# Performance work log

Hardware: AMD Instinct MI355X
Metric: run time of the kernel (lower is better)

The kernel has to match this reference:

```python
import jax, jax.numpy as jnp
import numpy as np

EPS = 1e-6
N_HEADS = 128
QK_NOPE = 128
QK_ROPE = 64
KV_RANK = 512

def rmsnorm(x, gamma):
    var = jnp.mean(jnp.square(x), axis=-1, keepdims=True)
    return x * jax.lax.rsqrt(var + EPS) * gamma

def apply_rope(x, cos, sin):
    # x: [..., D], cos/sin broadcastable to x; rotate-half convention
    x1, x2 = jnp.split(x, 2, axis=-1)
    rot = jnp.concatenate([-x2, x1], axis=-1)
    return x * cos + rot * sin

def setup_inputs() -> dict:
    key = jax.random.key(0)
    ks = jax.random.split(key, 6)
    T, H = 4096, 7168
    inp = {
        "token_x": jax.random.normal(ks[0], (T, H), jnp.float32),
        "wq_a": jax.random.normal(ks[1], (H, 1536), jnp.float32) * 0.02,
        "wq_b": jax.random.normal(ks[2], (1536, N_HEADS * (QK_NOPE + QK_ROPE)), jnp.float32) * 0.02,
        "wkv": jax.random.normal(ks[3], (H, KV_RANK + QK_ROPE), jnp.float32) * 0.02,
        "rope_cos": jax.random.uniform(ks[4], (T, QK_ROPE), jnp.float32, -1.0, 1.0),
        "rope_sin": jax.random.uniform(ks[5], (T, QK_ROPE), jnp.float32, -1.0, 1.0),
        "gamma_cq": jnp.ones((1536,), jnp.float32),
        "gamma_ckv": jnp.ones((KV_RANK,), jnp.float32),
    }
    return inp

def reference(token_x, wq_a, wq_b, wkv, rope_cos, rope_sin, gamma_cq, gamma_ckv):
    T = token_x.shape[0]
    # Query path: down-proj -> RMSNorm -> up-proj -> split -> RoPE on rope part
    cq = rmsnorm(token_x @ wq_a, gamma_cq)                    # [T, 1536]
    q = (cq @ wq_b).reshape(T, N_HEADS, QK_NOPE + QK_ROPE)    # [T, H, 192]
    q_nope, q_rope = q[..., :QK_NOPE], q[..., QK_NOPE:]
    q_rope = apply_rope(q_rope, rope_cos[:, None, :], rope_sin[:, None, :])
    query = jnp.concatenate([q_nope, q_rope], axis=-1)        # [T, H, 192]
    # KV path: joint down-proj -> split latent / rope-key -> RMSNorm + RoPE
    kv = token_x @ wkv                                        # [T, 576]
    ckv = rmsnorm(kv[:, :KV_RANK], gamma_ckv)                 # [T, 512]
    k_rope = apply_rope(kv[:, KV_RANK:], rope_cos, rope_sin)  # [T, 64]
    # Pack outputs into a single array: [T, H*192 + 512 + 64]
    return jnp.concatenate([query.reshape(T, -1), ckv, k_rope], axis=-1)
```

## Files before the change

kernel.cpp:

```cpp
#include <hip/hip_runtime.h>


typedef __attribute__((ext_vector_type(8))) __bf16 bf16x8;
typedef __attribute__((ext_vector_type(4))) float f32x4;

#define OUT_LD 25152

__device__ __forceinline__ unsigned short f2bf(float f) {
  union { float f; unsigned u; } v; v.f = f;
  unsigned r = v.u + 0x7FFFu + ((v.u >> 16) & 1u);
  return (unsigned short)(r >> 16);
}

__device__ __forceinline__ void gload16(const void* g, void* l) {
  __builtin_amdgcn_global_load_lds(
      (__attribute__((address_space(1))) void*)(void*)g,
      (__attribute__((address_space(3))) void*)l, 16, 0, 0);
}

__global__ void cvt_bf16(const float* __restrict__ in, unsigned short* __restrict__ out) {
  size_t i = (size_t)blockIdx.x * 256 + threadIdx.x;
  float4 f = ((const float4*)in)[i];
  ushort4 o;
  o.x = f2bf(f.x); o.y = f2bf(f.y); o.z = f2bf(f.z); o.w = f2bf(f.w);
  ((ushort4*)out)[i] = o;
}

__global__ void transpose_cvt(const float* __restrict__ in, unsigned short* __restrict__ out,
                              int K, int N, int Npad) {
  __shared__ float tile[32][33];
  int k0 = blockIdx.x * 32, n0 = blockIdx.y * 32;
  int tx = threadIdx.x, ty = threadIdx.y;
#pragma unroll
  for (int i = 0; i < 4; ++i) {
    int k = k0 + ty + i * 8;
    int n = n0 + tx;
    tile[ty + i * 8][tx] = (n < N) ? in[(size_t)k * N + n] : 0.f;
  }
  __syncthreads();
#pragma unroll
  for (int i = 0; i < 4; ++i) {
    int n = n0 + ty + i * 8;
    int k = k0 + tx;
    if (n < Npad) out[(size_t)n * K + k] = f2bf(tile[tx][ty + i * 8]);
  }
}

__global__ __launch_bounds__(512, 2) void gemm256(
    const unsigned short* __restrict__ A, const unsigned short* __restrict__ B,
    float* __restrict__ C, int K, int ldc, int Mtiles,
    const float* __restrict__ cs, const float* __restrict__ sn, int rope) {
  __shared__ __attribute__((aligned(128))) char lds[131072];
  const int tid = threadIdx.x;
  const int lane = tid & 63;
  const int wr = (tid >> 6) >> 2;
  const int wc = (tid >> 6) & 3;
  const int NT = K >> 6;

  const int nwg = gridDim.x;
  const int per = nwg >> 3;
  const int bid = blockIdx.x;
  const int swz = (bid & 7) * per + (bid >> 3);
  const int bm = swz % Mtiles, bn = swz / Mtiles;

  const int strow = tid >> 3;
  const int stcolb = (((tid & 7) ^ ((tid >> 3) & 7)) << 4);
  const size_t abase = (size_t)(bm * 256) * K;
  const size_t bbase = (size_t)(bn * 256) * K;

  f32x4 acc[2][2][4][2];
  const f32x4 z4 = {0.f, 0.f, 0.f, 0.f};
#pragma unroll
  for (int a = 0; a < 2; ++a)
#pragma unroll
    for (int b = 0; b < 2; ++b)
#pragma unroll
      for (int c = 0; c < 4; ++c)
#pragma unroll
        for (int d = 0; d < 2; ++d) acc[a][b][c][d] = z4;

#define STAGE_A(kt, bsel, u)                                                          \
  do {                                                                                \
    int row_ = (u) * 64 + strow;                                                      \
    gload16((const char*)(A + abase + (size_t)row_ * K + (size_t)(kt) * 64) + stcolb, \
            lds + (bsel) * 65536 + (u) * 8192 + tid * 16);                            \
  } while (0)
#define STAGE_B(kt, bsel, u)                                                          \
  do {                                                                                \
    int lrow_ = (u) * 64 + strow;                                                     \
    int n_ = ((lrow_ >> 5) & 3) * 64 + ((lrow_ >> 7) & 1) * 32 + (lrow_ & 31);        \
    gload16((const char*)(B + bbase + (size_t)n_ * K + (size_t)(kt) * 64) + stcolb,   \
            lds + (bsel) * 65536 + 32768 + (u) * 8192 + tid * 16);                    \
  } while (0)

#define READ_A(dst, QM, LBASE)                                              \
  do {                                                                      \
    _Pragma("unroll") for (int mf = 0; mf < 4; ++mf)                        \
        _Pragma("unroll") for (int ks = 0; ks < 2; ++ks) {                  \
      int row_ = (QM) * 128 + wr * 64 + mf * 16 + (lane & 15);              \
      int in_ = (ks * 64 + ((lane >> 4) << 4)) ^ ((row_ & 7) << 4);         \
      dst[mf][ks] = *(const bf16x8*)((LBASE) + row_ * 128 + in_);           \
    }                                                                       \
  } while (0)
#define READ_B(dst, QN, LBASE)                                              \
  do {                                                                      \
    _Pragma("unroll") for (int nf = 0; nf < 2; ++nf)                        \
        _Pragma("unroll") for (int ks = 0; ks < 2; ++ks) {                  \
      int c_ = wc * 64 + (QN) * 32 + nf * 16 + (lane & 15);                 \
      int rr_ = ((c_ >> 5) & 1) * 128 + ((c_ >> 6) & 3) * 32 + (c_ & 31);   \
      int in_ = (ks * 64 + ((lane >> 4) << 4)) ^ ((rr_ & 7) << 4);          \
      dst[nf][ks] = *(const bf16x8*)((LBASE) + 32768 + rr_ * 128 + in_);    \
    }                                                                       \
  } while (0)
#define MFMA_Q(QM, QN, AF, BB)                                              \
  do {                                                                      \
    __builtin_amdgcn_s_setprio(1);                                          \
    _Pragma("unroll") for (int mf = 0; mf < 4; ++mf)                        \
        _Pragma("unroll") for (int nf = 0; nf < 2; ++nf)                    \
            _Pragma("unroll") for (int ks = 0; ks < 2; ++ks)                \
                acc[QM][QN][mf][nf] = __builtin_amdgcn_mfma_f32_16x16x32_bf16( \
                    AF[mf][ks], BB[nf][ks], acc[QM][QN][mf][nf], 0, 0, 0);  \
    __builtin_amdgcn_s_setprio(0);                                          \
  } while (0)

  STAGE_A(0, 0, 0); STAGE_A(0, 0, 1); STAGE_A(0, 0, 2); STAGE_A(0, 0, 3);
  STAGE_B(0, 0, 0); STAGE_B(0, 0, 1); STAGE_B(0, 0, 2); STAGE_B(0, 0, 3);
  asm volatile("s_waitcnt vmcnt(0)" ::: "memory");
  __builtin_amdgcn_s_barrier();
  __builtin_amdgcn_sched_barrier(0);

  bf16x8 af0[4][2], af1[4][2], bb0[2][2], bb1[2][2];

  for (int t = 0; t < NT; ++t) {
    const int buf = t & 1;
    const int pb = buf ^ 1;
    const char* Lb = lds + buf * 65536;

    if (t + 1 < NT) {
      STAGE_A(t + 1, pb, 0); STAGE_A(t + 1, pb, 1);
      STAGE_A(t + 1, pb, 2); STAGE_A(t + 1, pb, 3);
      STAGE_B(t + 1, pb, 0); STAGE_B(t + 1, pb, 1);
      STAGE_B(t + 1, pb, 2); STAGE_B(t + 1, pb, 3);
    }
    __builtin_amdgcn_sched_barrier(0);

    READ_A(af0, 0, Lb);
    READ_B(bb0, 0, Lb);
    __builtin_amdgcn_sched_barrier(0);
    READ_B(bb1, 1, Lb);
    __builtin_amdgcn_sched_barrier(0);
    READ_A(af1, 1, Lb);
    __builtin_amdgcn_sched_barrier(0);

    asm volatile("s_waitcnt lgkmcnt(12)" ::: "memory");
    __builtin_amdgcn_sched_barrier(0);
    MFMA_Q(0, 0, af0, bb0);

    asm volatile("s_waitcnt lgkmcnt(8)" ::: "memory");
    __builtin_amdgcn_sched_barrier(0);
    MFMA_Q(0, 1, af0, bb1);

    asm volatile("s_waitcnt lgkmcnt(0)" ::: "memory");
    __builtin_amdgcn_sched_barrier(0);
    MFMA_Q(1, 1, af1, bb1);
    MFMA_Q(1, 0, af1, bb0);

    asm volatile("s_waitcnt vmcnt(0)" ::: "memory");
    __builtin_amdgcn_s_barrier();
    __builtin_amdgcn_sched_barrier(0);
  }

  const int colbase = bn * 256 + wc * 64;
  const int rbase = bm * 256 + wr * 64 + ((lane >> 4) << 2);
  const bool isrope = rope && ((colbase % 192) == 128);
  if (isrope) {
#pragma unroll
    for (int qm = 0; qm < 2; ++qm)
#pragma unroll
      for (int mf = 0; mf < 4; ++mf)
#pragma unroll
        for (int nf = 0; nf < 2; ++nf) {
          int i_ = nf * 16 + (lane & 15);
#pragma unroll
          for (int r = 0; r < 4; ++r) {
            int trow = rbase + qm * 128 + mf * 16 + r;
            float c1 = cs[trow * 64 + i_], s1 = sn[trow * 64 + i_];
            float c2 = cs[trow * 64 + 32 + i_], s2 = sn[trow * 64 + 32 + i_];
            float a = acc[qm][0][mf][nf][r], b = acc[qm][1][mf][nf][r];
            C[(size_t)trow * ldc + colbase + i_] = a * c1 - b * s1;
            C[(size_t)trow * ldc + colbase + 32 + i_] = b * c2 + a * s2;
          }
        }
  } else {
#pragma unroll
    for (int qm = 0; qm < 2; ++qm)
#pragma unroll
      for (int qn = 0; qn < 2; ++qn)
#pragma unroll
        for (int mf = 0; mf < 4; ++mf)
#pragma unroll
          for (int nf = 0; nf < 2; ++nf)
#pragma unroll
            for (int r = 0; r < 4; ++r) {
              int trow = rbase + qm * 128 + mf * 16 + r;
              C[(size_t)trow * ldc + colbase + qn * 32 + nf * 16 + (lane & 15)] =
                  acc[qm][qn][mf][nf][r];
            }
  }
#undef MFMA_Q
#undef READ_B
#undef READ_A
#undef STAGE_B
#undef STAGE_A
}

__global__ __launch_bounds__(256, 2) void gemm128(
    const unsigned short* __restrict__ A, const unsigned short* __restrict__ B,
    float* __restrict__ C, int K, int ldc, int Nvalid) {
  __shared__ __attribute__((aligned(128))) unsigned short As[128 * 32];
  __shared__ __attribute__((aligned(128))) unsigned short Bs[128 * 32];
  const int tid = threadIdx.x;
  const int lane = tid & 63;
  const int wid = tid >> 6;
  const int wr = wid >> 1, wc = wid & 1;
  const int bm = blockIdx.y, bn = blockIdx.x;
  const size_t abase = (size_t)bm * 128 * K;
  const size_t bbase = (size_t)bn * 128 * K;

  f32x4 acc[4][4];
  const f32x4 zero4 = {0.f, 0.f, 0.f, 0.f};
#pragma unroll
  for (int m = 0; m < 4; ++m)
#pragma unroll
    for (int n = 0; n < 4; ++n) acc[m][n] = zero4;

  const int r0 = tid >> 2;
  const int c0 = (tid & 3) * 8;

  for (int k0 = 0; k0 < K; k0 += 32) {
    gload16(A + abase + (size_t)r0 * K + k0 + c0, As + tid * 8);
    gload16(A + abase + (size_t)(r0 + 64) * K + k0 + c0, As + (256 + tid) * 8);
    gload16(B + bbase + (size_t)r0 * K + k0 + c0, Bs + tid * 8);
    gload16(B + bbase + (size_t)(r0 + 64) * K + k0 + c0, Bs + (256 + tid) * 8);
    __syncthreads();
    bf16x8 af[4], bfr[4];
#pragma unroll
    for (int m = 0; m < 4; ++m)
      af[m] = *(const bf16x8*)(As + (wr * 64 + m * 16 + (lane & 15)) * 32 + (lane >> 4) * 8);
#pragma unroll
    for (int n = 0; n < 4; ++n)
      bfr[n] = *(const bf16x8*)(Bs + (wc * 64 + n * 16 + (lane & 15)) * 32 + (lane >> 4) * 8);
#pragma unroll
    for (int m = 0; m < 4; ++m)
#pragma unroll
      for (int n = 0; n < 4; ++n)
        acc[m][n] = __builtin_amdgcn_mfma_f32_16x16x32_bf16(af[m], bfr[n], acc[m][n], 0, 0, 0);
    __syncthreads();
  }

  const int crow0 = bm * 128 + wr * 64 + ((lane >> 4) << 2);
  const int ccol0 = bn * 128 + wc * 64 + (lane & 15);
#pragma unroll
  for (int m = 0; m < 4; ++m) {
#pragma unroll
    for (int n = 0; n < 4; ++n) {
      int col = ccol0 + n * 16;
      if (col < Nvalid) {
#pragma unroll
        for (int r = 0; r < 4; ++r) {
          int row = crow0 + m * 16 + r;
          C[(size_t)row * ldc + col] = acc[m][n][r];
        }
      }
    }
  }
}

__global__ void rmsnorm_cq(const float* __restrict__ raw, const float* __restrict__ gamma,
                           unsigned short* __restrict__ out) {
  __shared__ float red[4];
  int t = blockIdx.x, tid = threadIdx.x;
  const float* r = raw + (size_t)t * 2176;
  float v[6];
  float ss = 0.f;
#pragma unroll
  for (int i = 0; i < 6; ++i) {
    v[i] = r[tid + i * 256];
    ss += v[i] * v[i];
  }
#pragma unroll
  for (int o = 32; o > 0; o >>= 1) ss += __shfl_xor(ss, o, 64);
  if ((tid & 63) == 0) red[tid >> 6] = ss;
  __syncthreads();
  ss = red[0] + red[1] + red[2] + red[3];
  float sc = rsqrtf(ss * (1.f / 1536.f) + 1e-6f);
#pragma unroll
  for (int i = 0; i < 6; ++i)
    out[(size_t)t * 1536 + tid + i * 256] = f2bf(v[i] * sc * gamma[tid + i * 256]);
}

__global__ void kv_epi(const float* __restrict__ raw, const float* __restrict__ gamma,
                       const float* __restrict__ cs, const float* __restrict__ sn,
                       float* __restrict__ out) {
  __shared__ float red[4];
  int t = blockIdx.x, tid = threadIdx.x;
  const float* r = raw + (size_t)t * 2176 + 1536;
  float v0 = r[tid], v1 = r[tid + 256];
  float ss = v0 * v0 + v1 * v1;
#pragma unroll
  for (int o = 32; o > 0; o >>= 1) ss += __shfl_xor(ss, o, 64);
  if ((tid & 63) == 0) red[tid >> 6] = ss;
  __syncthreads();
  ss = red[0] + red[1] + red[2] + red[3];
  float sc = rsqrtf(ss * (1.f / 512.f) + 1e-6f);
  float* orow = out + (size_t)t * OUT_LD + 24576;
  orow[tid] = v0 * sc * gamma[tid];
  orow[tid + 256] = v1 * sc * gamma[tid + 256];
  if (tid < 32) {
    float a = r[512 + tid], b = r[544 + tid];
    orow[512 + tid] = a * cs[t * 64 + tid] - b * sn[t * 64 + tid];
    orow[544 + tid] = b * cs[t * 64 + 32 + tid] + a * sn[t * 64 + 32 + tid];
  }
}

extern "C" void kernel_launch(void* const* d_in, const int* in_sizes, int n_in,
                              void* d_out, int out_size, void* d_ws, size_t ws_size,
                              hipStream_t stream) {
  const float* token_x = (const float*)d_in[0];
  const float* wq_a = (const float*)d_in[1];
  const float* wq_b = (const float*)d_in[2];
  const float* wkv = (const float*)d_in[3];
  const float* rope_cos = (const float*)d_in[4];
  const float* rope_sin = (const float*)d_in[5];
  const float* gamma_cq = (const float*)d_in[6];
  const float* gamma_ckv = (const float*)d_in[7];
  float* out = (float*)d_out;

  char* ws = (char*)d_ws;
  unsigned short* txb = (unsigned short*)ws;
  unsigned short* wqbT = (unsigned short*)(ws + 58720256);
  unsigned short* Bc = (unsigned short*)(ws + 134217728);
  float* raw = (float*)(ws + 165412864);
  unsigned short* cqb = (unsigned short*)(ws + 201064448);

  cvt_bf16<<<28672, 256, 0, stream>>>(token_x, txb);
  transpose_cvt<<<dim3(7168 / 32, 1536 / 32), dim3(32, 8), 0, stream>>>(wq_a, Bc, 7168, 1536, 1536);
  transpose_cvt<<<dim3(7168 / 32, 640 / 32), dim3(32, 8), 0, stream>>>(
      wkv, Bc + (size_t)1536 * 7168, 7168, 576, 640);
  transpose_cvt<<<dim3(1536 / 32, 24576 / 32), dim3(32, 8), 0, stream>>>(wq_b, wqbT, 1536, 24576, 24576);

  gemm128<<<dim3(17, 32), 256, 0, stream>>>(txb, Bc, raw, 7168, 2176, 2176);

  rmsnorm_cq<<<4096, 256, 0, stream>>>(raw, gamma_cq, cqb);
  kv_epi<<<4096, 256, 0, stream>>>(raw, gamma_ckv, rope_cos, rope_sin, out);

  gemm256<<<1536, 512, 0, stream>>>(cqb, wqbT, out, 1536, OUT_LD, 16, rope_cos, rope_sin, 1);
}
```

Before: 697.6 us.

## Fuse cq and kv RMSNorm epilogues and simplify gemm256 main-loop scheduling

Merges the two per-token RMSNorm/RoPE epilogue kernels into one launch that reads each raw row once, saving a launch and a second pass over the row. It also strips the hand-placed sched_barriers, partial lgkmcnt waits and explicit vmcnt/s_barrier from the gemm256 main loop, replacing them with __syncthreads and one setprio region around all MFMAs. That hands instruction interleaving back to the compiler, which may lose the hand-tuned overlap of LDS reads and MFMAs in the dominant GEMM.

```diff
diff --git a/kernel.cpp b/kernel.cpp
--- a/kernel.cpp
+++ b/kernel.cpp
@@ -114,20 +114,16 @@
   } while (0)
 #define MFMA_Q(QM, QN, AF, BB)                                              \
   do {                                                                      \
-    __builtin_amdgcn_s_setprio(1);                                          \
     _Pragma("unroll") for (int mf = 0; mf < 4; ++mf)                        \
         _Pragma("unroll") for (int nf = 0; nf < 2; ++nf)                    \
             _Pragma("unroll") for (int ks = 0; ks < 2; ++ks)                \
                 acc[QM][QN][mf][nf] = __builtin_amdgcn_mfma_f32_16x16x32_bf16( \
                     AF[mf][ks], BB[nf][ks], acc[QM][QN][mf][nf], 0, 0, 0);  \
-    __builtin_amdgcn_s_setprio(0);                                          \
   } while (0)
 
   STAGE_A(0, 0, 0); STAGE_A(0, 0, 1); STAGE_A(0, 0, 2); STAGE_A(0, 0, 3);
   STAGE_B(0, 0, 0); STAGE_B(0, 0, 1); STAGE_B(0, 0, 2); STAGE_B(0, 0, 3);
-  asm volatile("s_waitcnt vmcnt(0)" ::: "memory");
-  __builtin_amdgcn_s_barrier();
-  __builtin_amdgcn_sched_barrier(0);
+  __syncthreads();
 
   bf16x8 af0[4][2], af1[4][2], bb0[2][2], bb1[2][2];
 
@@ -142,32 +138,20 @@
       STAGE_B(t + 1, pb, 0); STAGE_B(t + 1, pb, 1);
       STAGE_B(t + 1, pb, 2); STAGE_B(t + 1, pb, 3);
     }
-    __builtin_amdgcn_sched_barrier(0);
 
     READ_A(af0, 0, Lb);
     READ_B(bb0, 0, Lb);
-    __builtin_amdgcn_sched_barrier(0);
     READ_B(bb1, 1, Lb);
-    __builtin_amdgcn_sched_barrier(0);
     READ_A(af1, 1, Lb);
-    __builtin_amdgcn_sched_barrier(0);
-
-    asm volatile("s_waitcnt lgkmcnt(12)" ::: "memory");
-    __builtin_amdgcn_sched_barrier(0);
+
+    __builtin_amdgcn_s_setprio(1);
     MFMA_Q(0, 0, af0, bb0);
-
-    asm volatile("s_waitcnt lgkmcnt(8)" ::: "memory");
-    __builtin_amdgcn_sched_barrier(0);
     MFMA_Q(0, 1, af0, bb1);
-
-    asm volatile("s_waitcnt lgkmcnt(0)" ::: "memory");
-    __builtin_amdgcn_sched_barrier(0);
     MFMA_Q(1, 1, af1, bb1);
     MFMA_Q(1, 0, af1, bb0);
-
-    asm volatile("s_waitcnt vmcnt(0)" ::: "memory");
-    __builtin_amdgcn_s_barrier();
-    __builtin_amdgcn_sched_barrier(0);
+    __builtin_amdgcn_s_setprio(0);
+
+    __syncthreads();
   }
 
   const int colbase = bn * 256 + wc * 64;
@@ -276,8 +260,10 @@
   }
 }
 
-__global__ void rmsnorm_cq(const float* __restrict__ raw, const float* __restrict__ gamma,
-                           unsigned short* __restrict__ out) {
+__global__ void epi1(const float* __restrict__ raw, const float* __restrict__ gcq,
+                     const float* __restrict__ gckv, const float* __restrict__ cs,
+                     const float* __restrict__ sn, unsigned short* __restrict__ cqb,
+                     float* __restrict__ out) {
   __shared__ float red[4];
   int t = blockIdx.x, tid = threadIdx.x;
   const float* r = raw + (size_t)t * 2176;
@@ -296,28 +282,21 @@
   float sc = rsqrtf(ss * (1.f / 1536.f) + 1e-6f);
 #pragma unroll
   for (int i = 0; i < 6; ++i)
-    out[(size_t)t * 1536 + tid + i * 256] = f2bf(v[i] * sc * gamma[tid + i * 256]);
-}
-
-__global__ void kv_epi(const float* __restrict__ raw, const float* __restrict__ gamma,
-                       const float* __restrict__ cs, const float* __restrict__ sn,
-                       float* __restrict__ out) {
-  __shared__ float red[4];
-  int t = blockIdx.x, tid = threadIdx.x;
-  const float* r = raw + (size_t)t * 2176 + 1536;
-  float v0 = r[tid], v1 = r[tid + 256];
-  float ss = v0 * v0 + v1 * v1;
-#pragma unroll
-  for (int o = 32; o > 0; o >>= 1) ss += __shfl_xor(ss, o, 64);
-  if ((tid & 63) == 0) red[tid >> 6] = ss;
-  __syncthreads();
-  ss = red[0] + red[1] + red[2] + red[3];
-  float sc = rsqrtf(ss * (1.f / 512.f) + 1e-6f);
+    cqb[(size_t)t * 1536 + tid + i * 256] = f2bf(v[i] * sc * gcq[tid + i * 256]);
+  float v0 = r[1536 + tid], v1 = r[1792 + tid];
+  float s2 = v0 * v0 + v1 * v1;
+#pragma unroll
+  for (int o = 32; o > 0; o >>= 1) s2 += __shfl_xor(s2, o, 64);
+  __syncthreads();
+  if ((tid & 63) == 0) red[tid >> 6] = s2;
+  __syncthreads();
+  s2 = red[0] + red[1] + red[2] + red[3];
+  float sck = rsqrtf(s2 * (1.f / 512.f) + 1e-6f);
   float* orow = out + (size_t)t * OUT_LD + 24576;
-  orow[tid] = v0 * sc * gamma[tid];
-  orow[tid + 256] = v1 * sc * gamma[tid + 256];
+  orow[tid] = v0 * sck * gckv[tid];
+  orow[tid + 256] = v1 * sck * gckv[tid + 256];
   if (tid < 32) {
-    float a = r[512 + tid], b = r[544 + tid];
+    float a = r[2048 + tid], b = r[2080 + tid];
     orow[512 + tid] = a * cs[t * 64 + tid] - b * sn[t * 64 + tid];
     orow[544 + tid] = b * cs[t * 64 + 32 + tid] + a * sn[t * 64 + 32 + tid];
   }
@@ -351,8 +330,7 @@
 
   gemm128<<<dim3(17, 32), 256, 0, stream>>>(txb, Bc, raw, 7168, 2176, 2176);
 
-  rmsnorm_cq<<<4096, 256, 0, stream>>>(raw, gamma_cq, cqb);
-  kv_epi<<<4096, 256, 0, stream>>>(raw, gamma_ckv, rope_cos, rope_sin, out);
+  epi1<<<4096, 256, 0, stream>>>(raw, gamma_cq, gamma_ckv, rope_cos, rope_sin, cqb, out);
 
   gemm256<<<1536, 512, 0, stream>>>(cqb, wqbT, out, 1536, OUT_LD, 16, rope_cos, rope_sin, 1);
 }
```

Result: no change. 684.1 us (-1.9%).
